# Kernel optimization log

Measured on AMD Instinct MI355X. Metric: run time of the kernel, lower is better.

Reference implementation:

```python
import jax, jax.numpy as jnp
import numpy as np

N_NODES = 50000
N_EDGES = 800000
NODE_DIM = 128
EDGE_DIM = 64
MSG_DIM = 128
IN_DIM = 2 * NODE_DIM + EDGE_DIM  # 320
LN_EPS = 1e-5


def setup_inputs() -> dict:
    key = jax.random.key(0)
    ks = jax.random.split(key, 12)
    nodes = jax.random.normal(ks[0], (N_NODES, NODE_DIM), dtype=jnp.float32)
    edge_index = jax.random.randint(ks[1], (2, N_EDGES), 0, N_NODES, dtype=jnp.int64)
    edges = jax.random.normal(ks[2], (N_EDGES, EDGE_DIM), dtype=jnp.float32)
    # query projection (kaiming-normal weight, zero bias)
    Wq = jax.random.normal(ks[3], (IN_DIM, MSG_DIM), dtype=jnp.float32) * np.sqrt(2.0 / IN_DIM)
    bq = jnp.zeros((MSG_DIM,), dtype=jnp.float32)
    # logit MLP: Linear(IN_DIM->MSG_DIM) -> ReLU -> LayerNorm -> Linear(MSG_DIM->1) -> ReLU
    W1 = jax.random.normal(ks[4], (IN_DIM, MSG_DIM), dtype=jnp.float32) * np.sqrt(1.0 / IN_DIM)
    b1 = jnp.zeros((MSG_DIM,), dtype=jnp.float32)
    gamma = jnp.ones((MSG_DIM,), dtype=jnp.float32)
    beta = jnp.zeros((MSG_DIM,), dtype=jnp.float32)
    W2 = jax.random.normal(ks[5], (MSG_DIM, 1), dtype=jnp.float32) * np.sqrt(1.0 / MSG_DIM)
    b2 = jnp.zeros((1,), dtype=jnp.float32)
    return {"nodes": nodes, "edge_index": edge_index, "edges": edges,
            "Wq": Wq, "bq": bq, "W1": W1, "b1": b1,
            "gamma": gamma, "beta": beta, "W2": W2, "b2": b2}


def _layernorm(h, gamma, beta):
    mu = jnp.mean(h, axis=-1, keepdims=True)
    var = jnp.mean(jnp.square(h - mu), axis=-1, keepdims=True)
    return (h - mu) / jnp.sqrt(var + LN_EPS) * gamma + beta


def _forward(nodes, edges, Wq, bq, W1, b1, gamma, beta, W2, b2, senders, receivers):
    n_nodes = nodes.shape[0]
    x = jnp.concatenate([nodes[senders], nodes[receivers], edges], axis=-1)  # (E, IN_DIM)
    queries = x @ Wq + bq                                                    # (E, MSG_DIM)
    h = jax.nn.relu(x @ W1 + b1)
    h = _layernorm(h, gamma, beta)
    logits = jax.nn.relu(h @ W2 + b2)[:, 0]                                  # (E,)
    # segment softmax over receivers
    seg_max = jax.ops.segment_max(logits, receivers, num_segments=n_nodes)
    seg_max = jnp.where(jnp.isfinite(seg_max), seg_max, 0.0)
    exp_l = jnp.exp(logits - seg_max[receivers])
    seg_sum = jax.ops.segment_sum(exp_l, receivers, num_segments=n_nodes)
    weights = exp_l / (seg_sum[receivers] + 1e-10)                           # (E,)
    messages = queries * weights[:, None]
    out = jax.ops.segment_sum(messages, receivers, num_segments=n_nodes)    # (N, MSG_DIM)
    return jax.nn.leaky_relu(out, negative_slope=0.01)


def reference(nodes, edge_index, edges, Wq, bq, W1, b1, gamma, beta, W2, b2):
    senders, receivers = edge_index[0], edge_index[1]
    return _forward(nodes, edges, Wq, bq, W1, b1, gamma, beta, W2, b2, senders, receivers)
```

## Files before the change

kernel.cpp:

```cpp
#include <hip/hip_runtime.h>
#include <hip/hip_bf16.h>

#define NN 50000
#define NE 800000
#define D 128
#define ED 64
#define IN_DIM 320
#define MB 64
#define KP 328
#define NT (NE / MB)
#define PGRID 512
#define NB ((NN + 255) / 256)

typedef short short8 __attribute__((ext_vector_type(8)));
typedef float f32x4 __attribute__((ext_vector_type(4)));

__device__ __forceinline__ ushort f2b(float f) {
  __hip_bfloat16 h = __float2bfloat16(f);
  return *reinterpret_cast<ushort*>(&h);
}
__device__ __forceinline__ float b2f(ushort u) {
  return __uint_as_float(((uint)u) << 16);
}
__device__ __forceinline__ ushort4 c4(float4 v) {
  ushort4 u; u.x = f2b(v.x); u.y = f2b(v.y); u.z = f2b(v.z); u.w = f2b(v.w);
  return u;
}

__device__ __forceinline__ void gather_regs(
    ushort4 g[20], const int* __restrict__ senders,
    const int* __restrict__ receivers, const float* __restrict__ nodes,
    const float* __restrict__ efeat, int e0, int tid)
{
  const int e = tid >> 2, p = tid & 3;
  const float* ns = nodes + (size_t)senders[e0 + e] * D;
  const float* nr = nodes + (size_t)receivers[e0 + e] * D;
  const float* ef = efeat + (size_t)(e0 + e) * ED;
#pragma unroll
  for (int i = 0; i < 8; ++i) g[i] = c4(*(const float4*)(ns + (p + 4 * i) * 4));
#pragma unroll
  for (int i = 0; i < 8; ++i) g[8 + i] = c4(*(const float4*)(nr + (p + 4 * i) * 4));
#pragma unroll
  for (int i = 0; i < 4; ++i) g[16 + i] = c4(*(const float4*)(ef + (p + 4 * i) * 4));
}

__device__ __forceinline__ void write_xs(
    ushort xs[MB][KP], const ushort4 g[20], int tid)
{
  const int e = tid >> 2, p = tid & 3;
#pragma unroll
  for (int i = 0; i < 8; ++i)
    *reinterpret_cast<ushort4*>(&xs[e][(p + 4 * i) * 4]) = g[i];
#pragma unroll
  for (int i = 0; i < 8; ++i)
    *reinterpret_cast<ushort4*>(&xs[e][128 + (p + 4 * i) * 4]) = g[8 + i];
#pragma unroll
  for (int i = 0; i < 4; ++i)
    *reinterpret_cast<ushort4*>(&xs[e][256 + (p + 4 * i) * 4]) = g[16 + i];
}

__global__ __launch_bounds__(256) void k_wconv(
    const float* __restrict__ Wq, const float* __restrict__ W1,
    ushort* __restrict__ Wqt, ushort* __restrict__ W1t)
{
  int i = blockIdx.x * 256 + threadIdx.x;
  if (i < D * IN_DIM) {
    int n = i / IN_DIM, k = i - n * IN_DIM;
    Wqt[i] = f2b(Wq[k * D + n]);
    W1t[i] = f2b(W1[k * D + n]);
  }
}

__global__ __launch_bounds__(256, 2) void k_fused(
    const float* __restrict__ nodes,
    const int* __restrict__ senders, const int* __restrict__ receivers,
    const float* __restrict__ efeat,
    const ushort* __restrict__ Wqt, const float* __restrict__ bq,
    const ushort* __restrict__ W1t, const float* __restrict__ b1,
    const float* __restrict__ gamma_, const float* __restrict__ beta_,
    const float* __restrict__ W2, const float* __restrict__ b2,
    ushort* __restrict__ queries, float* __restrict__ logits,
    float* __restrict__ seg_max)
{
  __shared__ ushort xs[MB][KP];
  __shared__ float red[MB][4][3];
  const int tid = threadIdx.x;
  const int w = tid >> 6, l = tid & 63, lr = l & 15, lg = l >> 4;
  const int n0 = 32 * w + lr, n1 = 32 * w + 16 + lr;

  const float b1a = b1[n0], b1b = b1[n1];
  const float g0 = gamma_[n0], g1 = gamma_[n1];
  const float be0 = beta_[n0], be1 = beta_[n1];
  const float w20 = W2[n0], w21 = W2[n1];
  const float bq0 = bq[n0], bq1 = bq[n1];
  const float b2s = b2[0];
  const float wg0 = w20 * g0, wg1 = w21 * g1;

  {
    float p1 = wg0 + wg1;
    float p2 = w20 * be0 + w21 * be1;
#pragma unroll
    for (int off = 1; off < 64; off <<= 1) {
      p1 += __shfl_xor(p1, off);
      p2 += __shfl_xor(p2, off);
    }
    if (l == 0) { red[0][w][0] = p1; red[0][w][1] = p2; }
  }
  __syncthreads();
  const float S1  = 0.25f * (red[0][0][0] + red[0][1][0] + red[0][2][0] + red[0][3][0]);
  const float B2t = 0.25f * (red[0][0][1] + red[0][1][1] + red[0][2][1] + red[0][3][1]) + b2s;

  int tile = blockIdx.x;
  ushort4 g[20];
  gather_regs(g, senders, receivers, nodes, efeat, tile * MB, tid);

  while (tile < NT) {
    const int e0 = tile * MB;
    write_xs(xs, g, tid);
    __syncthreads();

    f32x4 aq[4][2] = {};
#pragma unroll 2
    for (int ks = 0; ks < 10; ++ks) {
      short8 Q0 = *reinterpret_cast<const short8*>(Wqt + n0 * IN_DIM + ks * 32 + lg * 8);
      short8 Q1 = *reinterpret_cast<const short8*>(Wqt + n1 * IN_DIM + ks * 32 + lg * 8);
      short8 A[4];
#pragma unroll
      for (int mt = 0; mt < 4; ++mt)
        A[mt] = *reinterpret_cast<const short8*>(&xs[mt * 16 + lr][ks * 32 + lg * 8]);
#pragma unroll
      for (int mt = 0; mt < 4; ++mt) {
        aq[mt][0] = __builtin_amdgcn_mfma_f32_16x16x32_bf16(A[mt], Q0, aq[mt][0], 0, 0, 0);
        aq[mt][1] = __builtin_amdgcn_mfma_f32_16x16x32_bf16(A[mt], Q1, aq[mt][1], 0, 0, 0);
      }
    }
#pragma unroll
    for (int mt = 0; mt < 4; ++mt)
#pragma unroll
      for (int r = 0; r < 4; ++r) {
        int row = mt * 16 + lg * 4 + r;
        queries[(size_t)(e0 + row) * D + n0] = f2b(aq[mt][0][r] + bq0);
        queries[(size_t)(e0 + row) * D + n1] = f2b(aq[mt][1][r] + bq1);
      }

    const int nxt = tile + PGRID;
    if (nxt < NT)
      gather_regs(g, senders, receivers, nodes, efeat, nxt * MB, tid);

    f32x4 ah[4][2] = {};
#pragma unroll
    for (int ks = 0; ks < 10; ++ks) {
      short8 Y0 = *reinterpret_cast<const short8*>(W1t + n0 * IN_DIM + ks * 32 + lg * 8);
      short8 Y1 = *reinterpret_cast<const short8*>(W1t + n1 * IN_DIM + ks * 32 + lg * 8);
      short8 A[4];
#pragma unroll
      for (int mt = 0; mt < 4; ++mt)
        A[mt] = *reinterpret_cast<const short8*>(&xs[mt * 16 + lr][ks * 32 + lg * 8]);
#pragma unroll
      for (int mt = 0; mt < 4; ++mt) {
        ah[mt][0] = __builtin_amdgcn_mfma_f32_16x16x32_bf16(A[mt], Y0, ah[mt][0], 0, 0, 0);
        ah[mt][1] = __builtin_amdgcn_mfma_f32_16x16x32_bf16(A[mt], Y1, ah[mt][1], 0, 0, 0);
      }
    }

#pragma unroll
    for (int mt = 0; mt < 4; ++mt)
#pragma unroll
      for (int r = 0; r < 4; ++r) {
        float h0 = fmaxf(ah[mt][0][r] + b1a, 0.f);
        float h1 = fmaxf(ah[mt][1][r] + b1b, 0.f);
        float s = h0 + h1;
        float q = h0 * h0 + h1 * h1;
        float t = h0 * wg0 + h1 * wg1;
#pragma unroll
        for (int off = 1; off < 16; off <<= 1) {
          s += __shfl_xor(s, off);
          q += __shfl_xor(q, off);
          t += __shfl_xor(t, off);
        }
        if (lr == mt * 4 + r) {
          int row = mt * 16 + lg * 4 + r;
          red[row][w][0] = s;
          red[row][w][1] = q;
          red[row][w][2] = t;
        }
      }
    __syncthreads();
    if (tid < MB) {
      float s = red[tid][0][0] + red[tid][1][0] + red[tid][2][0] + red[tid][3][0];
      float q = red[tid][0][1] + red[tid][1][1] + red[tid][2][1] + red[tid][3][1];
      float t = red[tid][0][2] + red[tid][1][2] + red[tid][2][2] + red[tid][3][2];
      float mu = s * (1.f / 128.f);
      float var = fmaxf(q * (1.f / 128.f) - mu * mu, 0.f);
      float rs = rsqrtf(var + 1e-5f);
      float logit = fmaxf(rs * (t - mu * S1) + B2t, 0.f);
      logits[e0 + tid] = logit;
      atomicMax((int*)&seg_max[receivers[e0 + tid]], __float_as_int(logit));
    }
    tile = nxt;
  }
}

__global__ __launch_bounds__(256) void k_hist(
    const int* __restrict__ receivers, int* __restrict__ deg)
{
  int e = blockIdx.x * 256 + threadIdx.x;
  if (e < NE) atomicAdd(&deg[receivers[e]], 1);
}

__global__ __launch_bounds__(256) void k_scan1(
    const int* __restrict__ deg, int* __restrict__ bsum)
{
  __shared__ int buf[256];
  int i = blockIdx.x * 256 + threadIdx.x;
  int v = (i < NN) ? deg[i] : 0;
  buf[threadIdx.x] = v;
  __syncthreads();
  for (int off = 128; off > 0; off >>= 1) {
    if (threadIdx.x < off) buf[threadIdx.x] += buf[threadIdx.x + off];
    __syncthreads();
  }
  if (threadIdx.x == 0) bsum[blockIdx.x] = buf[0];
}

__global__ __launch_bounds__(256) void k_scan2(
    const int* __restrict__ bsum, int* __restrict__ bpre, int* __restrict__ offs)
{
  __shared__ int buf[256];
  int t = threadIdx.x;
  int v = (t < NB) ? bsum[t] : 0;
  buf[t] = v;
  __syncthreads();
  for (int off = 1; off < 256; off <<= 1) {
    int x = (t >= off) ? buf[t - off] : 0;
    __syncthreads();
    buf[t] += x;
    __syncthreads();
  }
  if (t < NB) bpre[t] = buf[t] - v;
  if (t == 0) offs[NN] = NE;
}

__global__ __launch_bounds__(256) void k_scan3(
    const int* __restrict__ deg, const int* __restrict__ bpre,
    int* __restrict__ offs, int* __restrict__ cursor)
{
  __shared__ int buf[256];
  int t = threadIdx.x;
  int i = blockIdx.x * 256 + t;
  int v = (i < NN) ? deg[i] : 0;
  buf[t] = v;
  __syncthreads();
  for (int off = 1; off < 256; off <<= 1) {
    int x = (t >= off) ? buf[t - off] : 0;
    __syncthreads();
    buf[t] += x;
    __syncthreads();
  }
  if (i < NN) {
    int o = bpre[blockIdx.x] + buf[t] - v;
    offs[i] = o;
    cursor[i] = o;
  }
}

__global__ __launch_bounds__(256) void k_bucket(
    const int* __restrict__ receivers, int* __restrict__ cursor,
    int* __restrict__ ebuf)
{
  int e = blockIdx.x * 256 + threadIdx.x;
  if (e < NE) {
    int pos = atomicAdd(&cursor[receivers[e]], 1);
    ebuf[pos] = e;
  }
}

__global__ __launch_bounds__(256) void k_bsort(
    const int* __restrict__ offs, int* __restrict__ ebuf)
{
  int node = blockIdx.x * 256 + threadIdx.x;
  if (node >= NN) return;
  const int beg = offs[node], end = offs[node + 1];
  for (int i = beg + 1; i < end; ++i) {
    int v = ebuf[i];
    int j = i - 1;
    while (j >= beg && ebuf[j] > v) { ebuf[j + 1] = ebuf[j]; --j; }
    ebuf[j + 1] = v;
  }
}

__global__ __launch_bounds__(256) void k_out(
    const int* __restrict__ offs, const int* __restrict__ ebuf,
    const float* __restrict__ logits, const float* __restrict__ seg_max,
    const ushort* __restrict__ queries, float* __restrict__ out)
{
  int node = blockIdx.x * 8 + (threadIdx.x >> 5);
  if (node >= NN) return;
  const int cg = (threadIdx.x & 31) * 4;
  const int beg = offs[node], end = offs[node + 1];
  const float smax = seg_max[node];
  float a0 = 0.f, a1 = 0.f, a2 = 0.f, a3 = 0.f, den = 0.f;

  int i = beg;
  for (; i + 4 <= end; i += 4) {
    int e0 = ebuf[i], e1 = ebuf[i + 1], e2 = ebuf[i + 2], e3 = ebuf[i + 3];
    float l0 = logits[e0], l1 = logits[e1], l2 = logits[e2], l3 = logits[e3];
    ushort4 q0 = *reinterpret_cast<const ushort4*>(queries + (size_t)e0 * D + cg);
    ushort4 q1 = *reinterpret_cast<const ushort4*>(queries + (size_t)e1 * D + cg);
    ushort4 q2 = *reinterpret_cast<const ushort4*>(queries + (size_t)e2 * D + cg);
    ushort4 q3 = *reinterpret_cast<const ushort4*>(queries + (size_t)e3 * D + cg);
    float x0 = expf(l0 - smax), x1 = expf(l1 - smax);
    float x2 = expf(l2 - smax), x3 = expf(l3 - smax);
    a0 = fmaf(x0, b2f(q0.x), a0); a1 = fmaf(x0, b2f(q0.y), a1);
    a2 = fmaf(x0, b2f(q0.z), a2); a3 = fmaf(x0, b2f(q0.w), a3); den += x0;
    a0 = fmaf(x1, b2f(q1.x), a0); a1 = fmaf(x1, b2f(q1.y), a1);
    a2 = fmaf(x1, b2f(q1.z), a2); a3 = fmaf(x1, b2f(q1.w), a3); den += x1;
    a0 = fmaf(x2, b2f(q2.x), a0); a1 = fmaf(x2, b2f(q2.y), a1);
    a2 = fmaf(x2, b2f(q2.z), a2); a3 = fmaf(x2, b2f(q2.w), a3); den += x2;
    a0 = fmaf(x3, b2f(q3.x), a0); a1 = fmaf(x3, b2f(q3.y), a1);
    a2 = fmaf(x3, b2f(q3.z), a2); a3 = fmaf(x3, b2f(q3.w), a3); den += x3;
  }
  for (; i < end; ++i) {
    int e = ebuf[i];
    float ex = expf(logits[e] - smax);
    ushort4 q = *reinterpret_cast<const ushort4*>(queries + (size_t)e * D + cg);
    a0 = fmaf(ex, b2f(q.x), a0); a1 = fmaf(ex, b2f(q.y), a1);
    a2 = fmaf(ex, b2f(q.z), a2); a3 = fmaf(ex, b2f(q.w), a3);
    den += ex;
  }

  float inv = 1.f / (den + 1e-10f);
  float4 v;
  v.x = a0 * inv; v.y = a1 * inv; v.z = a2 * inv; v.w = a3 * inv;
  v.x = v.x > 0.f ? v.x : 0.01f * v.x;
  v.y = v.y > 0.f ? v.y : 0.01f * v.y;
  v.z = v.z > 0.f ? v.z : 0.01f * v.z;
  v.w = v.w > 0.f ? v.w : 0.01f * v.w;
  *reinterpret_cast<float4*>(out + (size_t)node * D + cg) = v;
}

extern "C" void kernel_launch(void* const* d_in, const int* in_sizes, int n_in,
                              void* d_out, int out_size, void* d_ws, size_t ws_size,
                              hipStream_t stream) {
  const float* nodes  = (const float*)d_in[0];
  const int*   eidx   = (const int*)d_in[1];
  const float* efeat  = (const float*)d_in[2];
  const float* Wq     = (const float*)d_in[3];
  const float* bq     = (const float*)d_in[4];
  const float* W1     = (const float*)d_in[5];
  const float* b1     = (const float*)d_in[6];
  const float* gamma_ = (const float*)d_in[7];
  const float* beta_  = (const float*)d_in[8];
  const float* W2     = (const float*)d_in[9];
  const float* b2     = (const float*)d_in[10];
  const int* senders   = eidx;
  const int* receivers = eidx + NE;

  float* ws       = (float*)d_ws;
  float* logits   = ws;
  float* seg_max  = ws + NE;
  int*   deg      = (int*)(seg_max + NN);
  int*   offs     = deg + NN;
  int*   cursor   = offs + NN + 1;
  int*   bsum     = cursor + NN;
  int*   bpre     = bsum + 256;
  int*   ebuf     = bpre + 256 + 3;
  ushort* Wqt     = (ushort*)(ebuf + NE);
  ushort* W1t     = Wqt + D * IN_DIM;
  ushort* queries = W1t + D * IN_DIM;

  hipMemsetAsync(seg_max, 0, NN * sizeof(float), stream);
  hipMemsetAsync(deg, 0, NN * sizeof(int), stream);

  k_wconv<<<(D * IN_DIM + 255) / 256, 256, 0, stream>>>(Wq, W1, Wqt, W1t);

  k_hist<<<(NE + 255) / 256, 256, 0, stream>>>(receivers, deg);
  k_scan1<<<NB, 256, 0, stream>>>(deg, bsum);
  k_scan2<<<1, 256, 0, stream>>>(bsum, bpre, offs);
  k_scan3<<<NB, 256, 0, stream>>>(deg, bpre, offs, cursor);
  k_bucket<<<(NE + 255) / 256, 256, 0, stream>>>(receivers, cursor, ebuf);
  k_bsort<<<NB, 256, 0, stream>>>(offs, ebuf);

  k_fused<<<PGRID, 256, 0, stream>>>(nodes, senders, receivers, efeat,
                                     Wqt, bq, W1t, b1, gamma_, beta_, W2, b2,
                                     queries, logits, seg_max);

  k_out<<<(NN + 7) / 8, 256, 0, stream>>>(offs, ebuf, logits, seg_max,
                                          queries, (float*)d_out);
}
```

Measured before the change: 527.6 us.

## Process edges in receiver-sorted order so outputs are contiguous per node

The fused MLP kernel now walks edges in the receiver-sorted permutation (ebuf), gathering features through that indirection. It writes queries and logits at sorted positions. The output kernel then reads queries and logits contiguously per node instead of through ebuf indirection, which replaces random 8-byte query reads with streaming ones. In exchange the edge-feature gather in the fused kernel becomes random, and the sorted receiver order may give better locality on receiver node rows and on the seg_max atomics.

```diff
diff --git a/kernel.cpp b/kernel.cpp
--- a/kernel.cpp
+++ b/kernel.cpp
@@ -28,14 +28,15 @@
 }
 
 __device__ __forceinline__ void gather_regs(
-    ushort4 g[20], const int* __restrict__ senders,
-    const int* __restrict__ receivers, const float* __restrict__ nodes,
-    const float* __restrict__ efeat, int e0, int tid)
+    ushort4 g[20], const int* __restrict__ eid,
+    const int* __restrict__ senders, const int* __restrict__ receivers,
+    const float* __restrict__ nodes, const float* __restrict__ efeat, int tid)
 {
   const int e = tid >> 2, p = tid & 3;
-  const float* ns = nodes + (size_t)senders[e0 + e] * D;
-  const float* nr = nodes + (size_t)receivers[e0 + e] * D;
-  const float* ef = efeat + (size_t)(e0 + e) * ED;
+  const int ge = eid[e];
+  const float* ns = nodes + (size_t)senders[ge] * D;
+  const float* nr = nodes + (size_t)receivers[ge] * D;
+  const float* ef = efeat + (size_t)ge * ED;
 #pragma unroll
   for (int i = 0; i < 8; ++i) g[i] = c4(*(const float4*)(ns + (p + 4 * i) * 4));
 #pragma unroll
@@ -74,7 +75,7 @@
 __global__ __launch_bounds__(256, 2) void k_fused(
     const float* __restrict__ nodes,
     const int* __restrict__ senders, const int* __restrict__ receivers,
-    const float* __restrict__ efeat,
+    const float* __restrict__ efeat, const int* __restrict__ ebuf,
     const ushort* __restrict__ Wqt, const float* __restrict__ bq,
     const ushort* __restrict__ W1t, const float* __restrict__ b1,
     const float* __restrict__ gamma_, const float* __restrict__ beta_,
@@ -112,7 +113,7 @@
 
   int tile = blockIdx.x;
   ushort4 g[20];
-  gather_regs(g, senders, receivers, nodes, efeat, tile * MB, tid);
+  gather_regs(g, ebuf + tile * MB, senders, receivers, nodes, efeat, tid);
 
   while (tile < NT) {
     const int e0 = tile * MB;
@@ -145,7 +146,7 @@
 
     const int nxt = tile + PGRID;
     if (nxt < NT)
-      gather_regs(g, senders, receivers, nodes, efeat, nxt * MB, tid);
+      gather_regs(g, ebuf + nxt * MB, senders, receivers, nodes, efeat, tid);
 
     f32x4 ah[4][2] = {};
 #pragma unroll
@@ -195,7 +196,8 @@
       float rs = rsqrtf(var + 1e-5f);
       float logit = fmaxf(rs * (t - mu * S1) + B2t, 0.f);
       logits[e0 + tid] = logit;
-      atomicMax((int*)&seg_max[receivers[e0 + tid]], __float_as_int(logit));
+      int ge = ebuf[e0 + tid];
+      atomicMax((int*)&seg_max[receivers[ge]], __float_as_int(logit));
     }
     tile = nxt;
   }
@@ -290,9 +292,9 @@
 }
 
 __global__ __launch_bounds__(256) void k_out(
-    const int* __restrict__ offs, const int* __restrict__ ebuf,
-    const float* __restrict__ logits, const float* __restrict__ seg_max,
-    const ushort* __restrict__ queries, float* __restrict__ out)
+    const int* __restrict__ offs, const float* __restrict__ logits,
+    const float* __restrict__ seg_max, const ushort* __restrict__ queries,
+    float* __restrict__ out)
 {
   int node = blockIdx.x * 8 + (threadIdx.x >> 5);
   if (node >= NN) return;
@@ -303,12 +305,11 @@
 
   int i = beg;
   for (; i + 4 <= end; i += 4) {
-    int e0 = ebuf[i], e1 = ebuf[i + 1], e2 = ebuf[i + 2], e3 = ebuf[i + 3];
-    float l0 = logits[e0], l1 = logits[e1], l2 = logits[e2], l3 = logits[e3];
-    ushort4 q0 = *reinterpret_cast<const ushort4*>(queries + (size_t)e0 * D + cg);
-    ushort4 q1 = *reinterpret_cast<const ushort4*>(queries + (size_t)e1 * D + cg);
-    ushort4 q2 = *reinterpret_cast<const ushort4*>(queries + (size_t)e2 * D + cg);
-    ushort4 q3 = *reinterpret_cast<const ushort4*>(queries + (size_t)e3 * D + cg);
+    float l0 = logits[i], l1 = logits[i + 1], l2 = logits[i + 2], l3 = logits[i + 3];
+    ushort4 q0 = *reinterpret_cast<const ushort4*>(queries + (size_t)i * D + cg);
+    ushort4 q1 = *reinterpret_cast<const ushort4*>(queries + (size_t)(i + 1) * D + cg);
+    ushort4 q2 = *reinterpret_cast<const ushort4*>(queries + (size_t)(i + 2) * D + cg);
+    ushort4 q3 = *reinterpret_cast<const ushort4*>(queries + (size_t)(i + 3) * D + cg);
     float x0 = expf(l0 - smax), x1 = expf(l1 - smax);
     float x2 = expf(l2 - smax), x3 = expf(l3 - smax);
     a0 = fmaf(x0, b2f(q0.x), a0); a1 = fmaf(x0, b2f(q0.y), a1);
@@ -321,9 +322,8 @@
     a2 = fmaf(x3, b2f(q3.z), a2); a3 = fmaf(x3, b2f(q3.w), a3); den += x3;
   }
   for (; i < end; ++i) {
-    int e = ebuf[i];
-    float ex = expf(logits[e] - smax);
-    ushort4 q = *reinterpret_cast<const ushort4*>(queries + (size_t)e * D + cg);
+    float ex = expf(logits[i] - smax);
+    ushort4 q = *reinterpret_cast<const ushort4*>(queries + (size_t)i * D + cg);
     a0 = fmaf(ex, b2f(q.x), a0); a1 = fmaf(ex, b2f(q.y), a1);
     a2 = fmaf(ex, b2f(q.z), a2); a3 = fmaf(ex, b2f(q.w), a3);
     den += ex;
@@ -381,10 +381,10 @@
   k_bucket<<<(NE + 255) / 256, 256, 0, stream>>>(receivers, cursor, ebuf);
   k_bsort<<<NB, 256, 0, stream>>>(offs, ebuf);
 
-  k_fused<<<PGRID, 256, 0, stream>>>(nodes, senders, receivers, efeat,
+  k_fused<<<PGRID, 256, 0, stream>>>(nodes, senders, receivers, efeat, ebuf,
                                      Wqt, bq, W1t, b1, gamma_, beta_, W2, b2,
                                      queries, logits, seg_max);
 
-  k_out<<<(NN + 7) / 8, 256, 0, stream>>>(offs, ebuf, logits, seg_max,
+  k_out<<<(NN + 7) / 8, 256, 0, stream>>>(offs, logits, seg_max,
                                           queries, (float*)d_out);
 }
```

Measured after the change: 525.9 us. No clear change (-0.3%).
